# Kernel optimization log

Measured on AMD Instinct MI355X. Metric: run time of the kernel, lower is better.

Reference implementation:

```python
import jax, jax.numpy as jnp
import numpy as np

C_IN = 4   # in_ch + 1 (homogeneous coordinate)
C_OUT = 31

def setup_inputs() -> dict:
    key = jax.random.key(0)
    k1, k2 = jax.random.split(key)
    N, H, W = 4, 512, 512
    coeff = jax.random.normal(k1, (N, C_IN * C_OUT, H, W), dtype=jnp.float32)
    full_res_input = jax.random.uniform(k2, (N, 3, H, W), dtype=jnp.float32)
    return {"coeff": coeff, "full_res_input": full_res_input}

def reference(coeff, full_res_input):
    N, _, H, W = full_res_input.shape
    # Append homogeneous ones channel: [N, 4, H, W]
    aug = jnp.ones((N, 1, H, W), dtype=full_res_input.dtype)
    x = jnp.concatenate([full_res_input, aug], axis=1)
    # torch's permute(0,2,3,1).reshape(N,H,W,c_in,c_out) splits the channel dim
    # c = i*c_out + o, which equals reshaping directly in NCHW layout:
    c = coeff.reshape(N, C_IN, C_OUT, H, W)
    # Per-pixel 1x4 @ 4x31 matmul, output in NCHW directly (no permutes needed)
    out = jnp.einsum('nihw,niohw->nohw', x, c)
    return out
```

## Files before the change

kernel.cpp:

```cpp
#include <hip/hip_runtime.h>


#define C_OUT 31

__global__ __launch_bounds__(256)
void ApplyCoeffs_23261542875222_kernel(const float4* __restrict__ coeff,
                                       const float4* __restrict__ inp,
                                       float4* __restrict__ out,
                                       int p4)
{
    int t = blockIdx.x * blockDim.x + threadIdx.x;
    int n = t / p4;
    int p = t - n * p4;

    const float4* in_n = inp + (size_t)n * 3 * p4;
    float4 r = in_n[p];
    float4 g = in_n[p + p4];
    float4 b = in_n[p + 2 * p4];

    const float4* co = coeff + (size_t)n * 4 * C_OUT * p4 + p;
    float4* on = out + (size_t)n * C_OUT * p4 + p;

    #pragma unroll 4
    for (int o = 0; o < C_OUT; ++o) {
        float4 c0 = co[(size_t)o * p4];
        float4 c1 = co[(size_t)(C_OUT + o) * p4];
        float4 c2 = co[(size_t)(2 * C_OUT + o) * p4];
        float4 c3 = co[(size_t)(3 * C_OUT + o) * p4];
        float4 v;
        v.x = r.x * c0.x + g.x * c1.x + b.x * c2.x + c3.x;
        v.y = r.y * c0.y + g.y * c1.y + b.y * c2.y + c3.y;
        v.z = r.z * c0.z + g.z * c1.z + b.z * c2.z + c3.z;
        v.w = r.w * c0.w + g.w * c1.w + b.w * c2.w + c3.w;
        on[(size_t)o * p4] = v;
    }
}

extern "C" void kernel_launch(void* const* d_in, const int* in_sizes, int n_in,
                              void* d_out, int out_size, void* d_ws, size_t ws_size,
                              hipStream_t stream) {
    const float* coeff = (const float*)d_in[0];
    const float* inp   = (const float*)d_in[1];
    float* out         = (float*)d_out;

    const int N = 4;
    const int HW = 512 * 512;
    const int P4 = HW / 4;
    const int total = N * P4;
    dim3 block(256);
    dim3 grid(total / 256);

    ApplyCoeffs_23261542875222_kernel<<<grid, block, 0, stream>>>(
        (const float4*)coeff, (const float4*)inp, (float4*)out, P4);
}
```

Measured before the change: 697.8 us.

## Split output channels across two grid rows and use nontemporal loads/stores

Adds a second grid dimension so each thread handles half of the 31 output channels, which doubles the number of threads and the memory-level parallelism. Coefficient loads and output stores become nontemporal to avoid polluting the cache with streaming data, and pointer increments replace the per-iteration index multiplies. The RGB inputs are now read twice, once per half, which is a small amount of extra traffic.

```diff
diff --git a/kernel.cpp b/kernel.cpp
--- a/kernel.cpp
+++ b/kernel.cpp
@@ -3,36 +3,45 @@
 
 #define C_OUT 31
 
+typedef float f4 __attribute__((ext_vector_type(4)));
+
 __global__ __launch_bounds__(256)
-void ApplyCoeffs_23261542875222_kernel(const float4* __restrict__ coeff,
-                                       const float4* __restrict__ inp,
-                                       float4* __restrict__ out,
+void ApplyCoeffs_23261542875222_kernel(const f4* __restrict__ coeff,
+                                       const f4* __restrict__ inp,
+                                       f4* __restrict__ out,
                                        int p4)
 {
     int t = blockIdx.x * blockDim.x + threadIdx.x;
     int n = t / p4;
     int p = t - n * p4;
+    int h = blockIdx.y;
 
-    const float4* in_n = inp + (size_t)n * 3 * p4;
-    float4 r = in_n[p];
-    float4 g = in_n[p + p4];
-    float4 b = in_n[p + 2 * p4];
+    const f4* in_n = inp + (size_t)n * 3 * p4;
+    f4 r = in_n[p];
+    f4 g = in_n[p + p4];
+    f4 b = in_n[p + 2 * p4];
 
-    const float4* co = coeff + (size_t)n * 4 * C_OUT * p4 + p;
-    float4* on = out + (size_t)n * C_OUT * p4 + p;
+    const int o0   = h ? 16 : 0;
+    const int ocnt = h ? 15 : 16;
+
+    const size_t s = (size_t)C_OUT * p4;
+    const f4* co = coeff + (size_t)n * 4 * s + (size_t)o0 * p4 + p;
+    f4*       on = out   + (size_t)n * s     + (size_t)o0 * p4 + p;
 
     #pragma unroll 4
-    for (int o = 0; o < C_OUT; ++o) {
-        float4 c0 = co[(size_t)o * p4];
-        float4 c1 = co[(size_t)(C_OUT + o) * p4];
-        float4 c2 = co[(size_t)(2 * C_OUT + o) * p4];
-        float4 c3 = co[(size_t)(3 * C_OUT + o) * p4];
-        float4 v;
-        v.x = r.x * c0.x + g.x * c1.x + b.x * c2.x + c3.x;
-        v.y = r.y * c0.y + g.y * c1.y + b.y * c2.y + c3.y;
-        v.z = r.z * c0.z + g.z * c1.z + b.z * c2.z + c3.z;
-        v.w = r.w * c0.w + g.w * c1.w + b.w * c2.w + c3.w;
-        on[(size_t)o * p4] = v;
+    for (int o = 0; o < ocnt; ++o) {
+        f4 c0 = __builtin_nontemporal_load(co);
+        f4 c1 = __builtin_nontemporal_load(co + s);
+        f4 c2 = __builtin_nontemporal_load(co + 2 * s);
+        f4 c3 = __builtin_nontemporal_load(co + 3 * s);
+        f4 v;
+        v[0] = fmaf(r[0], c0[0], fmaf(g[0], c1[0], fmaf(b[0], c2[0], c3[0])));
+        v[1] = fmaf(r[1], c0[1], fmaf(g[1], c1[1], fmaf(b[1], c2[1], c3[1])));
+        v[2] = fmaf(r[2], c0[2], fmaf(g[2], c1[2], fmaf(b[2], c2[2], c3[2])));
+        v[3] = fmaf(r[3], c0[3], fmaf(g[3], c1[3], fmaf(b[3], c2[3], c3[3])));
+        __builtin_nontemporal_store(v, on);
+        co += p4;
+        on += p4;
     }
 }
 
@@ -48,8 +57,8 @@
     const int P4 = HW / 4;
     const int total = N * P4;
     dim3 block(256);
-    dim3 grid(total / 256);
+    dim3 grid(total / 256, 2);
 
     ApplyCoeffs_23261542875222_kernel<<<grid, block, 0, stream>>>(
-        (const float4*)coeff, (const float4*)inp, (float4*)out, P4);
+        (const f4*)coeff, (const f4*)inp, (f4*)out, P4);
 }
```

Result: faster. 679.6 us (-2.6%).
